# Performance work log

Hardware: AMD Instinct MI355X
Metric: run time of the kernel (lower is better)

Reference implementation:

```python
import jax, jax.numpy as jnp
import numpy as np

V, E, S_MAX, H, L = 32000, 1024, 2048, 16, 6
D = E // H  # head_dim = 64
EPS = 1e-5


def _ln(x, g, b):
    mu = jnp.mean(x, axis=-1, keepdims=True)
    var = jnp.mean(jnp.square(x - mu), axis=-1, keepdims=True)
    return (x - mu) * jax.lax.rsqrt(var + EPS) * g + b


def setup_inputs() -> dict:
    key = jax.random.key(0)
    ks = iter(jax.random.split(key, 32))
    std = 0.02
    B, S = 1, 2048
    inp = {
        "tokens": jax.random.randint(next(ks), (B, S), 0, V, dtype=jnp.int32),
        "W_emb": jax.random.normal(next(ks), (V, E), jnp.float32) * std,  # tied with fc_out
        "W_pos": jax.random.normal(next(ks), (S_MAX, E), jnp.float32) * std,
        # per-layer stacked params [L, ...]
        "Wq": jax.random.normal(next(ks), (L, E, E), jnp.float32) * std,
        "Wk": jax.random.normal(next(ks), (L, E, E), jnp.float32) * std,
        "Wv": jax.random.normal(next(ks), (L, E, E), jnp.float32) * std,
        "Wo": jax.random.normal(next(ks), (L, E, E), jnp.float32) * std,
        "bo": jnp.zeros((L, E), jnp.float32),
        "ln1_g": jnp.ones((L, E), jnp.float32),
        "ln1_b": jnp.zeros((L, E), jnp.float32),
        "ln2_g": jnp.ones((L, E), jnp.float32),
        "ln2_b": jnp.zeros((L, E), jnp.float32),
        "W1": jax.random.normal(next(ks), (L, 4 * E, E), jnp.float32) * std,
        "b1": jnp.zeros((L, 4 * E), jnp.float32),
        "W2": jax.random.normal(next(ks), (L, E, 4 * E), jnp.float32) * std,
        "b2": jnp.zeros((L, E), jnp.float32),
        "lnf_g": jnp.ones((E,), jnp.float32),
        "lnf_b": jnp.zeros((E,), jnp.float32),
    }
    return inp


def _gpt_forward(tokens, W_emb, W_pos, Wq, Wk, Wv, Wo, bo, ln1_g, ln1_b,
                 ln2_g, ln2_b, W1, b1, W2, b2, lnf_g, lnf_b):
    B, S = tokens.shape
    x = W_emb[tokens] + W_pos[:S][None, :, :]  # [B,S,E]
    causal = jnp.tril(jnp.ones((S, S), bool))  # [S,S]
    scale = 1.0 / np.sqrt(D)

    def block(x, p):
        wq, wk, wv, wo, bo_, g1, b1n, g2, b2n, w1, bf1, w2, bf2 = p
        h = _ln(x, g1, b1n)
        # torch Linear: y = x @ W.T ; split heads -> [B,H,S,D]
        def heads(w):
            return (h @ w.T).reshape(B, S, H, D).transpose(0, 2, 1, 3)
        q, k, v = heads(wq), heads(wk), heads(wv)
        scores = jnp.einsum('bhqd,bhkd->bhqk', q, k) * scale
        scores = jnp.where(causal[None, None], scores, -jnp.inf)
        attn = jax.nn.softmax(scores, axis=-1)
        o = jnp.einsum('bhqk,bhkd->bhqd', attn, v)
        o = o.transpose(0, 2, 1, 3).reshape(B, S, E)
        x = x + o @ wo.T + bo_
        h2 = _ln(x, g2, b2n)
        ff = jax.nn.gelu(h2 @ w1.T + bf1, approximate=False) @ w2.T + bf2
        return x + ff, None

    params = (Wq, Wk, Wv, Wo, bo, ln1_g, ln1_b, ln2_g, ln2_b, W1, b1, W2, b2)
    x, _ = jax.lax.scan(block, x, params)
    x = _ln(x, lnf_g, lnf_b)
    return x @ W_emb.T  # tied output projection [B,S,V]


def reference(tokens, W_emb, W_pos, Wq, Wk, Wv, Wo, bo, ln1_g, ln1_b,
              ln2_g, ln2_b, W1, b1, W2, b2, lnf_g, lnf_b):
    return _gpt_forward(tokens, W_emb, W_pos, Wq, Wk, Wv, Wo, bo, ln1_g,
                        ln1_b, ln2_g, ln2_b, W1, b1, W2, b2, lnf_g, lnf_b)
```

## Files before the change

### kernel.cpp

```cpp
#include <hip/hip_runtime.h>
#include <math.h>

#define S_LEN 2048
#define EMB 1024
#define NHEAD 16
#define HDIM 64
#define NLAYER 6
#define VOCAB 32000
#define FFDIM 4096

using f32x4 = __attribute__((ext_vector_type(4))) float;
using bf16x8 = __attribute__((ext_vector_type(8))) __bf16;
typedef unsigned short us;

static __device__ __forceinline__ unsigned short f2bf(float f) {
  union { float f; unsigned int u; } v; v.f = f;
  unsigned int r = v.u + 0x7FFFu + ((v.u >> 16) & 1u);
  return (unsigned short)(r >> 16);
}

#define GLOAD_LDS16(g, l)                                                      \
  __builtin_amdgcn_global_load_lds(                                            \
      (const __attribute__((address_space(1))) void*)(g),                      \
      (__attribute__((address_space(3))) void*)(l), 16, 0, 0)

__global__ __launch_bounds__(256) void cvt_bf16_kernel(
    const float* __restrict__ in, us* __restrict__ out, long n) {
  long i = ((long)blockIdx.x * 256 + threadIdx.x) * 8;
  if (i >= n) return;
  const float4* p = (const float4*)(in + i);
  float4 a = p[0], b = p[1];
  uint4 o;
  o.x = (unsigned)f2bf(a.x) | ((unsigned)f2bf(a.y) << 16);
  o.y = (unsigned)f2bf(a.z) | ((unsigned)f2bf(a.w) << 16);
  o.z = (unsigned)f2bf(b.x) | ((unsigned)f2bf(b.y) << 16);
  o.w = (unsigned)f2bf(b.z) | ((unsigned)f2bf(b.w) << 16);
  *(uint4*)(out + i) = o;
}

__global__ __launch_bounds__(256) void embed_kernel(
    const int* __restrict__ tok, const float* __restrict__ Wemb,
    const float* __restrict__ Wpos, float* __restrict__ x) {
  int s = blockIdx.x, t = threadIdx.x;
  int tk = tok[s];
  const float4* we = (const float4*)(Wemb + (size_t)tk * EMB);
  const float4* wp = (const float4*)(Wpos + (size_t)s * EMB);
  float4 a = we[t], b = wp[t];
  float4 o; o.x = a.x + b.x; o.y = a.y + b.y; o.z = a.z + b.z; o.w = a.w + b.w;
  ((float4*)(x + (size_t)s * EMB))[t] = o;
}

__global__ __launch_bounds__(256) void ln_kernel(
    const float* __restrict__ x, const float* __restrict__ g,
    const float* __restrict__ b, us* __restrict__ out) {
  int row = blockIdx.x, t = threadIdx.x, lane = t & 63, wave = t >> 6;
  float4 v = ((const float4*)(x + (size_t)row * EMB))[t];
  float s = v.x + v.y + v.z + v.w;
  float q = v.x * v.x + v.y * v.y + v.z * v.z + v.w * v.w;
  #pragma unroll
  for (int d = 1; d < 64; d <<= 1) { s += __shfl_xor(s, d); q += __shfl_xor(q, d); }
  __shared__ float rs[4], rq[4];
  if (lane == 0) { rs[wave] = s; rq[wave] = q; }
  __syncthreads();
  s = rs[0] + rs[1] + rs[2] + rs[3];
  q = rq[0] + rq[1] + rq[2] + rq[3];
  float mean = s * (1.0f / EMB);
  float var = q * (1.0f / EMB) - mean * mean;
  float rstd = rsqrtf(var + 1e-5f);
  float4 gg = ((const float4*)g)[t], bb = ((const float4*)b)[t];
  ushort4 o;
  o.x = f2bf((v.x - mean) * rstd * gg.x + bb.x);
  o.y = f2bf((v.y - mean) * rstd * gg.y + bb.y);
  o.z = f2bf((v.z - mean) * rstd * gg.z + bb.z);
  o.w = f2bf((v.w - mean) * rstd * gg.w + bb.w);
  ((ushort4*)(out + (size_t)row * EMB))[t] = o;
}

template <int SK>
__global__ __launch_bounds__(256) void reduce_ln_kernel(
    float* __restrict__ x, const float* __restrict__ p,
    const float* __restrict__ bias, const float* __restrict__ g,
    const float* __restrict__ b, us* __restrict__ out) {
  int row = blockIdx.x, t = threadIdx.x, lane = t & 63, wave = t >> 6;
  const size_t plane = (size_t)S_LEN * EMB;
  float4 v = ((const float4*)(x + (size_t)row * EMB))[t];
  float4 bb4 = ((const float4*)bias)[t];
  v.x += bb4.x; v.y += bb4.y; v.z += bb4.z; v.w += bb4.w;
  #pragma unroll
  for (int z = 0; z < SK; ++z) {
    float4 q4 = ((const float4*)(p + z * plane + (size_t)row * EMB))[t];
    v.x += q4.x; v.y += q4.y; v.z += q4.z; v.w += q4.w;
  }
  ((float4*)(x + (size_t)row * EMB))[t] = v;
  float s = v.x + v.y + v.z + v.w;
  float q = v.x * v.x + v.y * v.y + v.z * v.z + v.w * v.w;
  #pragma unroll
  for (int d = 1; d < 64; d <<= 1) { s += __shfl_xor(s, d); q += __shfl_xor(q, d); }
  __shared__ float rs[4], rq[4];
  if (lane == 0) { rs[wave] = s; rq[wave] = q; }
  __syncthreads();
  s = rs[0] + rs[1] + rs[2] + rs[3];
  q = rq[0] + rq[1] + rq[2] + rq[3];
  float mean = s * (1.0f / EMB);
  float var = q * (1.0f / EMB) - mean * mean;
  float rstd = rsqrtf(var + 1e-5f);
  float4 gg = ((const float4*)g)[t], lb = ((const float4*)b)[t];
  ushort4 o;
  o.x = f2bf((v.x - mean) * rstd * gg.x + lb.x);
  o.y = f2bf((v.y - mean) * rstd * gg.y + lb.y);
  o.z = f2bf((v.z - mean) * rstd * gg.z + lb.z);
  o.w = f2bf((v.w - mean) * rstd * gg.w + lb.w);
  ((ushort4*)(out + (size_t)row * EMB))[t] = o;
}

#define STAGE_R(MATP, BROW, LDSB, TT)                                          \
  {                                                                            \
    const int kk0 = (TT) << 5;                                                 \
    _Pragma("unroll")                                                          \
    for (int i_ = 0; i_ < 2; ++i_) {                                           \
      const int ci = t + i_ * 256;                                             \
      const int rr = ci >> 2, cc = ci & 3;                                     \
      const int src = (cc ^ ((rr >> 1) & 3)) * 8;                              \
      GLOAD_LDS16(MATP + (size_t)((BROW) + rr) * K + kk0 + src,                \
                  &LDSB[0] + (wave * 64 + i_ * 256) * 8);                      \
    }                                                                          \
  }

template <int HAS_BIAS, int DO_GELU, int OUT_BF16>
__global__ __launch_bounds__(256) void gemm_r128(
    const us* __restrict__ A, const us* __restrict__ B0,
    const us* __restrict__ B1, const us* __restrict__ B2,
    const float* __restrict__ bias,
    void* C0, void* C1, void* C2, int M, int N, int K) {
  const us* B = blockIdx.z == 0 ? B0 : (blockIdx.z == 1 ? B1 : B2);
  void* C = blockIdx.z == 0 ? C0 : (blockIdx.z == 1 ? C1 : C2);
  const int nwg = gridDim.x * gridDim.y;
  int lin = blockIdx.y * gridDim.x + blockIdx.x;
  {
    const int qx = nwg >> 3, r = nwg & 7;
    const int xcd = lin & 7, idx = lin >> 3;
    lin = (xcd < r ? xcd * (qx + 1) : r * (qx + 1) + (xcd - r) * qx) + idx;
  }
  const int m0 = (lin % gridDim.x) * 128, n0 = (lin / gridDim.x) * 128;
  const int t = threadIdx.x, lane = t & 63, wave = t >> 6;
  const int lq = lane & 15, hi = lane >> 4;
  const int wm = (wave >> 1) * 64, wn = (wave & 1) * 64;
  __shared__ __align__(16) us As[3][128 * 32];
  __shared__ __align__(16) us Bs[3][128 * 32];
  f32x4 acc[4][4] = {};
  const int nt = K >> 5;

  STAGE_R(A, m0, As[0], 0); STAGE_R(B, n0, Bs[0], 0);
  STAGE_R(A, m0, As[1], 1); STAGE_R(B, n0, Bs[1], 1);
  STAGE_R(A, m0, As[2], 2); STAGE_R(B, n0, Bs[2], 2);
  asm volatile("s_waitcnt vmcnt(8)" ::: "memory");
  __builtin_amdgcn_s_barrier();
  __builtin_amdgcn_sched_barrier(0);

  int bb = 0;
  for (int tt = 0; tt < nt; ++tt) {
    const int sb = (bb + 2 >= 3) ? bb - 1 : bb + 2;
    const us* Ab = &As[bb][0];
    const us* Bb = &Bs[bb][0];
    bf16x8 a[4], b[4];
    #pragma unroll
    for (int f = 0; f < 4; ++f) {
      const int row = wm + f * 16 + lq;
      a[f] = *(const bf16x8*)(Ab + row * 32 + ((hi ^ ((row >> 1) & 3)) * 8));
    }
    #pragma unroll
    for (int f = 0; f < 4; ++f) {
      const int row = wn + f * 16 + lq;
      b[f] = *(const bf16x8*)(Bb + row * 32 + ((hi ^ ((row >> 1) & 3)) * 8));
    }
    if (tt + 2 < nt) {
      STAGE_R(A, m0, As[sb], tt + 2);
      STAGE_R(B, n0, Bs[sb], tt + 2);
    }
    __builtin_amdgcn_s_setprio(1);
    #pragma unroll
    for (int i = 0; i < 4; ++i)
      #pragma unroll
      for (int j = 0; j < 4; ++j)
        acc[i][j] = __builtin_amdgcn_mfma_f32_16x16x32_bf16(a[i], b[j], acc[i][j], 0, 0, 0);
    __builtin_amdgcn_s_setprio(0);
    if (tt + 2 < nt) {
      asm volatile("s_waitcnt vmcnt(4)" ::: "memory");
    } else {
      asm volatile("s_waitcnt vmcnt(0)" ::: "memory");
    }
    __builtin_amdgcn_s_barrier();
    __builtin_amdgcn_sched_barrier(0);
    bb = (bb + 1 == 3) ? 0 : bb + 1;
  }
  const int r0 = hi * 4;
  #pragma unroll
  for (int i = 0; i < 4; ++i) {
    #pragma unroll
    for (int j = 0; j < 4; ++j) {
      const int col = n0 + wn + j * 16 + lq;
      float bv = HAS_BIAS ? bias[col] : 0.0f;
      #pragma unroll
      for (int r = 0; r < 4; ++r) {
        const int row = m0 + wm + i * 16 + r0 + r;
        float val = acc[i][j][r] + bv;
        if (DO_GELU) val = val * 0.5f * (1.0f + erff(val * 0.70710678118f));
        if (OUT_BF16) ((us*)C)[(size_t)row * N + col] = f2bf(val);
        else          ((float*)C)[(size_t)row * N + col] = val;
      }
    }
  }
}

__global__ __launch_bounds__(256) void gemm_rsk(
    const us* __restrict__ A, const us* __restrict__ B,
    float* __restrict__ C, int M, int N, int K, int kSlice) {
  const int z = blockIdx.z;
  const int nwg = gridDim.x * gridDim.y;
  int lin = blockIdx.y * gridDim.x + blockIdx.x;
  {
    const int qx = nwg >> 3, r = nwg & 7;
    const int xcd = lin & 7, idx = lin >> 3;
    lin = (xcd < r ? xcd * (qx + 1) : r * (qx + 1) + (xcd - r) * qx) + idx;
  }
  const int m0 = (lin % gridDim.x) * 128, n0 = (lin / gridDim.x) * 128;
  const int t = threadIdx.x, lane = t & 63, wave = t >> 6;
  const int lq = lane & 15, hi = lane >> 4;
  const int wm = (wave >> 1) * 64, wn = (wave & 1) * 64;
  __shared__ __align__(16) us As[3][128 * 32];
  __shared__ __align__(16) us Bs[3][128 * 32];
  f32x4 acc[4][4] = {};
  const int nt = kSlice >> 5;
  const int tb = z * (kSlice >> 5);

  STAGE_R(A, m0, As[0], tb + 0); STAGE_R(B, n0, Bs[0], tb + 0);
  STAGE_R(A, m0, As[1], tb + 1); STAGE_R(B, n0, Bs[1], tb + 1);
  STAGE_R(A, m0, As[2], tb + 2); STAGE_R(B, n0, Bs[2], tb + 2);
  asm volatile("s_waitcnt vmcnt(8)" ::: "memory");
  __builtin_amdgcn_s_barrier();
  __builtin_amdgcn_sched_barrier(0);

  int bb = 0;
  for (int tt = 0; tt < nt; ++tt) {
    const int sb = (bb + 2 >= 3) ? bb - 1 : bb + 2;
    const us* Ab = &As[bb][0];
    const us* Bb = &Bs[bb][0];
    bf16x8 a[4], b[4];
    #pragma unroll
    for (int f = 0; f < 4; ++f) {
      const int row = wm + f * 16 + lq;
      a[f] = *(const bf16x8*)(Ab + row * 32 + ((hi ^ ((row >> 1) & 3)) * 8));
    }
    #pragma unroll
    for (int f = 0; f < 4; ++f) {
      const int row = wn + f * 16 + lq;
      b[f] = *(const bf16x8*)(Bb + row * 32 + ((hi ^ ((row >> 1) & 3)) * 8));
    }
    if (tt + 2 < nt) {
      STAGE_R(A, m0, As[sb], tb + tt + 2);
      STAGE_R(B, n0, Bs[sb], tb + tt + 2);
    }
    __builtin_amdgcn_s_setprio(1);
    #pragma unroll
    for (int i = 0; i < 4; ++i)
      #pragma unroll
      for (int j = 0; j < 4; ++j)
        acc[i][j] = __builtin_amdgcn_mfma_f32_16x16x32_bf16(a[i], b[j], acc[i][j], 0, 0, 0);
    __builtin_amdgcn_s_setprio(0);
    if (tt + 2 < nt) {
      asm volatile("s_waitcnt vmcnt(4)" ::: "memory");
    } else {
      asm volatile("s_waitcnt vmcnt(0)" ::: "memory");
    }
    __builtin_amdgcn_s_barrier();
    __builtin_amdgcn_sched_barrier(0);
    bb = (bb + 1 == 3) ? 0 : bb + 1;
  }
  float* Cz = C + (size_t)z * M * N;
  #pragma unroll
  for (int i = 0; i < 4; ++i)
    #pragma unroll
    for (int j = 0; j < 4; ++j) {
      const int col = n0 + wn + j * 16 + lq;
      #pragma unroll
      for (int r = 0; r < 4; ++r)
        Cz[(size_t)(m0 + wm + i * 16 + hi * 4 + r) * N + col] = acc[i][j][r];
    }
}

__global__ __launch_bounds__(512, 1) void gemm_v8p(
    const us* __restrict__ A, const us* __restrict__ B,
    float* __restrict__ C, int M, int N, int K) {
  const int nwg = gridDim.x * gridDim.y;
  int lin = blockIdx.y * gridDim.x + blockIdx.x;
  {
    const int qx = nwg >> 3, r = nwg & 7;
    const int xcd = lin & 7, idx = lin >> 3;
    lin = (xcd < r ? xcd * (qx + 1) : r * (qx + 1) + (xcd - r) * qx) + idx;
  }
  const int m0 = (lin % gridDim.x) * 256, n0 = (lin / gridDim.x) * 256;
  const int t = threadIdx.x, lane = t & 63, wave = t >> 6;
  const int lq = lane & 15, hi = lane >> 4;
  const int rbase = (wave >> 2) * 128, cbase = (wave & 3) * 64;
  __shared__ __align__(16) us As[3][256 * 32];
  __shared__ __align__(16) us Bs[3][256 * 32];
  f32x4 acc[8][4] = {};
  const int nt = K >> 5;

#define STAGE_T(MAT, LDSB, TT)                                                 \
  {                                                                            \
    const int kk0 = (TT) << 5;                                                 \
    _Pragma("unroll")                                                          \
    for (int i_ = 0; i_ < 2; ++i_) {                                           \
      const int ci = t + i_ * 512;                                             \
      const int rr = ci >> 2, cc = ci & 3;                                     \
      const int src = (cc ^ ((rr >> 1) & 3)) * 8;                              \
      GLOAD_LDS16(MAT + (size_t)(((MAT == A) ? m0 : n0) + rr) * K + kk0 + src, \
                  &LDSB[0] + (wave * 64 + i_ * 512) * 8);                      \
    }                                                                          \
  }

  STAGE_T(A, As[0], 0); STAGE_T(B, Bs[0], 0);
  STAGE_T(A, As[1], 1); STAGE_T(B, Bs[1], 1);
  STAGE_T(A, As[2], 2); STAGE_T(B, Bs[2], 2);
  asm volatile("s_waitcnt vmcnt(8)" ::: "memory");
  __builtin_amdgcn_s_barrier();
  __builtin_amdgcn_sched_barrier(0);

  int bb = 0;
  for (int tt = 0; tt < nt; ++tt) {
    const int sb = (bb + 2 >= 3) ? bb - 1 : bb + 2;
    const us* Ab = &As[bb][0];
    const us* Bb = &Bs[bb][0];
    bf16x8 a0[4], a1[4], b0[4];
    #pragma unroll
    for (int f = 0; f < 4; ++f) {
      const int row = rbase + f * 16 + lq;
      a0[f] = *(const bf16x8*)(Ab + row * 32 + ((hi ^ ((row >> 1) & 3)) * 8));
    }
    #pragma unroll
    for (int f = 0; f < 4; ++f) {
      const int row = rbase + 64 + f * 16 + lq;
      a1[f] = *(const bf16x8*)(Ab + row * 32 + ((hi ^ ((row >> 1) & 3)) * 8));
    }
    #pragma unroll
    for (int f = 0; f < 4; ++f) {
      const int row = cbase + f * 16 + lq;
      b0[f] = *(const bf16x8*)(Bb + row * 32 + ((hi ^ ((row >> 1) & 3)) * 8));
    }
    if (tt + 2 < nt) {
      STAGE_T(A, As[sb], tt + 2);
      STAGE_T(B, Bs[sb], tt + 2);
    }
    __builtin_amdgcn_s_setprio(1);
    #pragma unroll
    for (int i = 0; i < 4; ++i)
      #pragma unroll
      for (int j = 0; j < 4; ++j)
        acc[i][j] = __builtin_amdgcn_mfma_f32_16x16x32_bf16(a0[i], b0[j], acc[i][j], 0, 0, 0);
    #pragma unroll
    for (int i = 0; i < 4; ++i)
      #pragma unroll
      for (int j = 0; j < 4; ++j)
        acc[4 + i][j] = __builtin_amdgcn_mfma_f32_16x16x32_bf16(a1[i], b0[j], acc[4 + i][j], 0, 0, 0);
    __builtin_amdgcn_s_setprio(0);
    if (tt + 2 < nt) {
      asm volatile("s_waitcnt vmcnt(4)" ::: "memory");
    } else {
      asm volatile("s_waitcnt vmcnt(0)" ::: "memory");
    }
    __builtin_amdgcn_s_barrier();
    __builtin_amdgcn_sched_barrier(0);
    bb = (bb + 1 == 3) ? 0 : bb + 1;
  }
#undef STAGE_T
  #pragma unroll
  for (int i = 0; i < 8; ++i)
    #pragma unroll
    for (int j = 0; j < 4; ++j) {
      const int col = n0 + cbase + j * 16 + lq;
      #pragma unroll
      for (int r = 0; r < 4; ++r)
        C[(size_t)(m0 + rbase + i * 16 + hi * 4 + r) * N + col] = acc[i][j][r];
    }
}

__global__ __launch_bounds__(256) void attn_kernel(
    const us* __restrict__ qb, const us* __restrict__ kb,
    const us* __restrict__ vb, us* __restrict__ ob) {
  const int qt = gridDim.x - 1 - blockIdx.x;
  const int head = blockIdx.y;
  const int t = threadIdx.x, lane = t & 63, wave = t >> 6;
  const int hi = lane >> 4, lq = lane & 15;
  const int hd = head * HDIM;
  const int q0w = qt * 64 + wave * 16;
  __shared__ __align__(16) us Kl[2][64 * 64];
  __shared__ __align__(16) us Vl[2][64 * 72];
  __shared__ __align__(16) us Pl[4][16][72];
  bf16x8 qf[2];
  {
    const us* qp = qb + (size_t)(q0w + lq) * EMB + hd + hi * 8;
    qf[0] = *(const bf16x8*)qp;
    qf[1] = *(const bf16x8*)(qp + 32);
    #pragma unroll
    for (int e = 0; e < 8; ++e) {
      qf[0][e] = (__bf16)((float)qf[0][e] * 0.125f);
      qf[1][e] = (__bf16)((float)qf[1][e] * 0.125f);
    }
  }
  f32x4 accO[4] = {};
  float m_run = -1e30f, l_run = 0.f;
  const int vr2 = (t >> 3) * 2, d8 = (t & 7) * 8;
  const int q_g = q0w + lq;

  {
    #pragma unroll
    for (int i = 0; i < 2; ++i) {
      const int c = wave * 64 + lane + i * 256;
      const int row = c >> 3, j = c & 7;
      const int colE = (j * 8) ^ ((row & 7) << 3);
      GLOAD_LDS16(kb + (size_t)(row) * EMB + hd + colE,
                  &Kl[0][0] + (wave * 64 + i * 256) * 8);
    }
    const us* vp = vb + (size_t)vr2 * EMB + hd + d8;
    uint4 vA = *(const uint4*)vp;
    uint4 vB = *(const uint4*)(vp + EMB);
    const unsigned* wa = (const unsigned*)&vA;
    const unsigned* wb = (const unsigned*)&vB;
    #pragma unroll
    for (int i = 0; i < 8; ++i) {
      unsigned lo = (i & 1) ? (wa[i >> 1] >> 16) : (wa[i >> 1] & 0xffffu);
      unsigned hw = (i & 1) ? (wb[i >> 1] >> 16) : (wb[i >> 1] & 0xffffu);
      *(unsigned*)(&Vl[0][0] + (d8 + i) * 72 + vr2) = lo | (hw << 16);
    }
  }
  __syncthreads();
  int cur = 0;
  for (int kt = 0; kt <= qt; ++kt) {
    uint4 vA, vB;
    if (kt < qt) {
      #pragma unroll
      for (int i = 0; i < 2; ++i) {
        const int c = wave * 64 + lane + i * 256;
        const int row = c >> 3, j = c & 7;
        const int colE = (j * 8) ^ ((row & 7) << 3);
        GLOAD_LDS16(kb + (size_t)((kt + 1) * 64 + row) * EMB + hd + colE,
                    &Kl[cur ^ 1][0] + (wave * 64 + i * 256) * 8);
      }
      const us* vp = vb + (size_t)((kt + 1) * 64 + vr2) * EMB + hd + d8;
      vA = *(const uint4*)vp;
      vB = *(const uint4*)(vp + EMB);
    }
    f32x4 sc[4] = {};
    #pragma unroll
    for (int ks = 0; ks < 2; ++ks) {
      #pragma unroll
      for (int fn = 0; fn < 4; ++fn) {
        const int rowk = fn * 16 + lq;
        const us* kp = &Kl[cur][0] + rowk * 64 + ((ks * 32 + hi * 8) ^ ((rowk & 7) << 3));
        sc[fn] = __builtin_amdgcn_mfma_f32_16x16x32_bf16(
            *(const bf16x8*)kp, qf[ks], sc[fn], 0, 0, 0);
      }
    }
    float pv[16];
    float pmax = -1e30f;
    if (kt == qt) {
      #pragma unroll
      for (int fn = 0; fn < 4; ++fn)
        #pragma unroll
        for (int r = 0; r < 4; ++r) {
          const int k_g = kt * 64 + fn * 16 + hi * 4 + r;
          float sv = sc[fn][r];
          if (k_g > q_g) sv = -1e30f;
          pv[fn * 4 + r] = sv;
          pmax = fmaxf(pmax, sv);
        }
    } else {
      #pragma unroll
      for (int fn = 0; fn < 4; ++fn)
        #pragma unroll
        for (int r = 0; r < 4; ++r) {
          float sv = sc[fn][r];
          pv[fn * 4 + r] = sv;
          pmax = fmaxf(pmax, sv);
        }
    }
    pmax = fmaxf(pmax, __shfl_xor(pmax, 16));
    pmax = fmaxf(pmax, __shfl_xor(pmax, 32));
    if (!__all(pmax <= m_run + 8.0f)) {
      const float mn = fmaxf(m_run, pmax);
      const float alpha = __expf(m_run - mn);
      m_run = mn;
      l_run *= alpha;
      float ar[4];
      #pragma unroll
      for (int r = 0; r < 4; ++r) ar[r] = __shfl(alpha, hi * 4 + r);
      #pragma unroll
      for (int df = 0; df < 4; ++df)
        #pragma unroll
        for (int r = 0; r < 4; ++r) accO[df][r] *= ar[r];
    }
    float rsum = 0.f;
    #pragma unroll
    for (int i = 0; i < 16; ++i) {
      float e = __expf(pv[i] - m_run);
      pv[i] = e;
      rsum += e;
    }
    rsum += __shfl_xor(rsum, 16);
    rsum += __shfl_xor(rsum, 32);
    l_run += rsum;
    #pragma unroll
    for (int fn = 0; fn < 4; ++fn) {
      ushort4 pk;
      pk.x = f2bf(pv[fn * 4 + 0]);
      pk.y = f2bf(pv[fn * 4 + 1]);
      pk.z = f2bf(pv[fn * 4 + 2]);
      pk.w = f2bf(pv[fn * 4 + 3]);
      *(ushort4*)&Pl[wave][lq][fn * 16 + hi * 4] = pk;
    }
    #pragma unroll
    for (int ks = 0; ks < 2; ++ks) {
      bf16x8 pf = *(const bf16x8*)&Pl[wave][lq][ks * 32 + hi * 8];
      #pragma unroll
      for (int df = 0; df < 4; ++df) {
        bf16x8 vf = *(const bf16x8*)(&Vl[cur][0] + (df * 16 + lq) * 72 + ks * 32 + hi * 8);
        accO[df] = __builtin_amdgcn_mfma_f32_16x16x32_bf16(pf, vf, accO[df], 0, 0, 0);
      }
    }
    if (kt < qt) {
      const unsigned* wa = (const unsigned*)&vA;
      const unsigned* wb = (const unsigned*)&vB;
      #pragma unroll
      for (int i = 0; i < 8; ++i) {
        unsigned lo = (i & 1) ? (wa[i >> 1] >> 16) : (wa[i >> 1] & 0xffffu);
        unsigned hw = (i & 1) ? (wb[i >> 1] >> 16) : (wb[i >> 1] & 0xffffu);
        *(unsigned*)(&Vl[cur ^ 1][0] + (d8 + i) * 72 + vr2) = lo | (hw << 16);
      }
    }
    __syncthreads();
    cur ^= 1;
  }
  float linv[4];
  #pragma unroll
  for (int r = 0; r < 4; ++r) linv[r] = 1.0f / __shfl(l_run, hi * 4 + r);
  #pragma unroll
  for (int r = 0; r < 4; ++r) {
    const int row = q0w + hi * 4 + r;
    #pragma unroll
    for (int df = 0; df < 4; ++df)
      ob[(size_t)row * EMB + hd + df * 16 + lq] = f2bf(accO[df][r] * linv[r]);
  }
}

extern "C" void kernel_launch(void* const* d_in, const int* in_sizes, int n_in,
                              void* d_out, int out_size, void* d_ws, size_t ws_size,
                              hipStream_t stream) {
  const int* tok = (const int*)d_in[0];
  const float* Wemb = (const float*)d_in[1];
  const float* Wpos = (const float*)d_in[2];
  const float* Wq = (const float*)d_in[3];
  const float* Wk = (const float*)d_in[4];
  const float* Wv = (const float*)d_in[5];
  const float* Wo = (const float*)d_in[6];
  const float* bo = (const float*)d_in[7];
  const float* ln1g = (const float*)d_in[8];
  const float* ln1b = (const float*)d_in[9];
  const float* ln2g = (const float*)d_in[10];
  const float* ln2b = (const float*)d_in[11];
  const float* W1 = (const float*)d_in[12];
  const float* b1 = (const float*)d_in[13];
  const float* W2 = (const float*)d_in[14];
  const float* b2 = (const float*)d_in[15];
  const float* lnfg = (const float*)d_in[16];
  const float* lnfb = (const float*)d_in[17];
  (void)in_sizes; (void)n_in; (void)out_size;

  const size_t MB = 1u << 20;
  char* ws = (char*)d_ws;
  float* x = (float*)ws;
  us* h  = (us*)(ws + 8 * MB);
  us* qb = (us*)(ws + 12 * MB);
  us* kb = (us*)(ws + 16 * MB);
  us* vb = (us*)(ws + 20 * MB);
  us* ob = (us*)(ws + 24 * MB);
  us* fb = (us*)(ws + 12 * MB);
  us* cWq = (us*)(ws + 28 * MB);
  us* cWk = (us*)(ws + 40 * MB);
  us* cWv = (us*)(ws + 52 * MB);
  us* cWo = (us*)(ws + 64 * MB);
  us* cW1 = (us*)(ws + 76 * MB);
  us* cW2 = (us*)(ws + 124 * MB);
  us* cWemb = (us*)(ws + 172 * MB);
  float* pbuf = (float*)(ws + 236 * MB);
  const size_t need = 236 * MB + 32 * MB;
  if (ws_size < need) {
    embed_kernel<<<dim3(S_LEN), 256, 0, stream>>>(tok, Wemb, Wpos, x);
    return;
  }

  embed_kernel<<<dim3(S_LEN), 256, 0, stream>>>(tok, Wemb, Wpos, x);

  const long nE2 = (long)NLAYER * EMB * EMB;
  const long nF  = (long)NLAYER * FFDIM * EMB;
  const long nV  = (long)VOCAB * EMB;
  cvt_bf16_kernel<<<(int)(nE2 / 2048), 256, 0, stream>>>(Wq, cWq, nE2);
  cvt_bf16_kernel<<<(int)(nE2 / 2048), 256, 0, stream>>>(Wk, cWk, nE2);
  cvt_bf16_kernel<<<(int)(nE2 / 2048), 256, 0, stream>>>(Wv, cWv, nE2);
  cvt_bf16_kernel<<<(int)(nE2 / 2048), 256, 0, stream>>>(Wo, cWo, nE2);
  cvt_bf16_kernel<<<(int)(nF / 2048), 256, 0, stream>>>(W1, cW1, nF);
  cvt_bf16_kernel<<<(int)(nF / 2048), 256, 0, stream>>>(W2, cW2, nF);
  cvt_bf16_kernel<<<(int)(nV / 2048), 256, 0, stream>>>(Wemb, cWemb, nV);

  ln_kernel<<<S_LEN, 256, 0, stream>>>(x, ln1g, ln1b, h);
  for (int l = 0; l < NLAYER; ++l) {
    const size_t wofs = (size_t)l * EMB * EMB;
    const size_t fofs = (size_t)l * FFDIM * EMB;
    gemm_r128<0, 0, 1><<<dim3(16, 8, 3), 256, 0, stream>>>(
        h, cWq + wofs, cWk + wofs, cWv + wofs, nullptr,
        qb, kb, vb, S_LEN, EMB, EMB);
    attn_kernel<<<dim3(32, NHEAD), 256, 0, stream>>>(qb, kb, vb, ob);
    gemm_rsk<<<dim3(16, 8, 2), 256, 0, stream>>>(
        ob, cWo + wofs, pbuf, S_LEN, EMB, EMB, EMB / 2);
    reduce_ln_kernel<2><<<S_LEN, 256, 0, stream>>>(
        x, pbuf, bo + l * EMB, ln2g + l * EMB, ln2b + l * EMB, h);
    gemm_r128<1, 1, 1><<<dim3(16, 32, 1), 256, 0, stream>>>(
        h, cW1 + fofs, nullptr, nullptr, b1 + l * FFDIM,
        fb, nullptr, nullptr, S_LEN, FFDIM, EMB);
    gemm_rsk<<<dim3(16, 8, 4), 256, 0, stream>>>(
        fb, cW2 + fofs, pbuf, S_LEN, EMB, FFDIM, FFDIM / 4);
    if (l < NLAYER - 1)
      reduce_ln_kernel<4><<<S_LEN, 256, 0, stream>>>(
          x, pbuf, b2 + l * EMB, ln1g + (l + 1) * EMB, ln1b + (l + 1) * EMB, h);
    else
      reduce_ln_kernel<4><<<S_LEN, 256, 0, stream>>>(
          x, pbuf, b2 + l * EMB, lnfg, lnfb, h);
  }
  gemm_v8p<<<dim3(8, 125), 512, 0, stream>>>(
      h, cWemb, (float*)d_out, S_LEN, VOCAB, EMB);
}
```

Before: 1.382 ms.

## Add 64-row QKV GEMM, use exp2 softmax, split Wo GEMM four ways

Adds a new gemm_r64 kernel with 64x128 tiles for the QKV projection, doubling the grid from 384 to 768 workgroups to fill the CUs better. In attention, the log2(e) factor is folded into the Q prescale so softmax can use exp2f instead of __expf. The Wo projection's split-K goes from 2 to 4 slices, with the matching reduce_ln variant. These aim to raise occupancy and parallelism, at the cost of more partial-sum traffic and less reuse per tile.

```diff
diff --git a/kernel.cpp b/kernel.cpp
--- a/kernel.cpp
+++ b/kernel.cpp
@@ -210,6 +210,107 @@
       }
     }
   }
+}
+
+__global__ __launch_bounds__(256) void gemm_r64(
+    const us* __restrict__ A, const us* __restrict__ B0,
+    const us* __restrict__ B1, const us* __restrict__ B2,
+    void* C0, void* C1, void* C2, int M, int N, int K) {
+  const us* B = blockIdx.z == 0 ? B0 : (blockIdx.z == 1 ? B1 : B2);
+  void* C = blockIdx.z == 0 ? C0 : (blockIdx.z == 1 ? C1 : C2);
+  const int nwg = gridDim.x * gridDim.y;
+  int lin = blockIdx.y * gridDim.x + blockIdx.x;
+  {
+    const int qx = nwg >> 3, r = nwg & 7;
+    const int xcd = lin & 7, idx = lin >> 3;
+    lin = (xcd < r ? xcd * (qx + 1) : r * (qx + 1) + (xcd - r) * qx) + idx;
+  }
+  const int m0 = (lin % gridDim.x) * 64, n0 = (lin / gridDim.x) * 128;
+  const int t = threadIdx.x, lane = t & 63, wave = t >> 6;
+  const int lq = lane & 15, hi = lane >> 4;
+  const int wm = (wave >> 1) * 32, wn = (wave & 1) * 64;
+  __shared__ __align__(16) us As[3][64 * 32];
+  __shared__ __align__(16) us Bs[3][128 * 32];
+  f32x4 acc[2][4] = {};
+  const int nt = K >> 5;
+
+#define STAGE_A64(LDSB, TT)                                                    \
+  {                                                                            \
+    const int kk0 = (TT) << 5;                                                 \
+    const int rr = t >> 2, cc = t & 3;                                         \
+    const int src = (cc ^ ((rr >> 1) & 3)) * 8;                                \
+    GLOAD_LDS16(A + (size_t)(m0 + rr) * K + kk0 + src,                         \
+                &LDSB[0] + (wave * 64) * 8);                                   \
+  }
+#define STAGE_B64(LDSB, TT)                                                    \
+  {                                                                            \
+    const int kk0 = (TT) << 5;                                                 \
+    _Pragma("unroll")                                                          \
+    for (int i_ = 0; i_ < 2; ++i_) {                                           \
+      const int ci = t + i_ * 256;                                             \
+      const int rr = ci >> 2, cc = ci & 3;                                     \
+      const int src = (cc ^ ((rr >> 1) & 3)) * 8;                              \
+      GLOAD_LDS16(B + (size_t)(n0 + rr) * K + kk0 + src,                       \
+                  &LDSB[0] + (wave * 64 + i_ * 256) * 8);                      \
+    }                                                                          \
+  }
+
+  STAGE_A64(As[0], 0); STAGE_B64(Bs[0], 0);
+  STAGE_A64(As[1], 1); STAGE_B64(Bs[1], 1);
+  STAGE_A64(As[2], 2); STAGE_B64(Bs[2], 2);
+  asm volatile("s_waitcnt vmcnt(6)" ::: "memory");
+  __builtin_amdgcn_s_barrier();
+  __builtin_amdgcn_sched_barrier(0);
+
+  int bb = 0;
+  for (int tt = 0; tt < nt; ++tt) {
+    const int sb = (bb + 2 >= 3) ? bb - 1 : bb + 2;
+    const us* Ab = &As[bb][0];
+    const us* Bb = &Bs[bb][0];
+    bf16x8 a[2], b[4];
+    #pragma unroll
+    for (int f = 0; f < 2; ++f) {
+      const int row = wm + f * 16 + lq;
+      a[f] = *(const bf16x8*)(Ab + row * 32 + ((hi ^ ((row >> 1) & 3)) * 8));
+    }
+    #pragma unroll
+    for (int f = 0; f < 4; ++f) {
+      const int row = wn + f * 16 + lq;
+      b[f] = *(const bf16x8*)(Bb + row * 32 + ((hi ^ ((row >> 1) & 3)) * 8));
+    }
+    if (tt + 2 < nt) {
+      STAGE_A64(As[sb], tt + 2);
+      STAGE_B64(Bs[sb], tt + 2);
+    }
+    __builtin_amdgcn_s_setprio(1);
+    #pragma unroll
+    for (int i = 0; i < 2; ++i)
+      #pragma unroll
+      for (int j = 0; j < 4; ++j)
+        acc[i][j] = __builtin_amdgcn_mfma_f32_16x16x32_bf16(a[i], b[j], acc[i][j], 0, 0, 0);
+    __builtin_amdgcn_s_setprio(0);
+    if (tt + 2 < nt) {
+      asm volatile("s_waitcnt vmcnt(3)" ::: "memory");
+    } else {
+      asm volatile("s_waitcnt vmcnt(0)" ::: "memory");
+    }
+    __builtin_amdgcn_s_barrier();
+    __builtin_amdgcn_sched_barrier(0);
+    bb = (bb + 1 == 3) ? 0 : bb + 1;
+  }
+#undef STAGE_A64
+#undef STAGE_B64
+  #pragma unroll
+  for (int i = 0; i < 2; ++i)
+    #pragma unroll
+    for (int j = 0; j < 4; ++j) {
+      const int col = n0 + wn + j * 16 + lq;
+      #pragma unroll
+      for (int r = 0; r < 4; ++r) {
+        const int row = m0 + wm + i * 16 + hi * 4 + r;
+        ((us*)C)[(size_t)row * N + col] = f2bf(acc[i][j][r]);
+      }
+    }
 }
 
 __global__ __launch_bounds__(256) void gemm_rsk(
@@ -404,8 +505,8 @@
     qf[1] = *(const bf16x8*)(qp + 32);
     #pragma unroll
     for (int e = 0; e < 8; ++e) {
-      qf[0][e] = (__bf16)((float)qf[0][e] * 0.125f);
-      qf[1][e] = (__bf16)((float)qf[1][e] * 0.125f);
+      qf[0][e] = (__bf16)((float)qf[0][e] * 0.18033688f);
+      qf[1][e] = (__bf16)((float)qf[1][e] * 0.18033688f);
     }
   }
   f32x4 accO[4] = {};
@@ -489,7 +590,7 @@
     pmax = fmaxf(pmax, __shfl_xor(pmax, 32));
     if (!__all(pmax <= m_run + 8.0f)) {
       const float mn = fmaxf(m_run, pmax);
-      const float alpha = __expf(m_run - mn);
+      const float alpha = exp2f(m_run - mn);
       m_run = mn;
       l_run *= alpha;
       float ar[4];
@@ -503,7 +604,7 @@
     float rsum = 0.f;
     #pragma unroll
     for (int i = 0; i < 16; ++i) {
-      float e = __expf(pv[i] - m_run);
+      float e = exp2f(pv[i] - m_run);
       pv[i] = e;
       rsum += e;
     }
@@ -616,13 +717,13 @@
   for (int l = 0; l < NLAYER; ++l) {
     const size_t wofs = (size_t)l * EMB * EMB;
     const size_t fofs = (size_t)l * FFDIM * EMB;
-    gemm_r128<0, 0, 1><<<dim3(16, 8, 3), 256, 0, stream>>>(
-        h, cWq + wofs, cWk + wofs, cWv + wofs, nullptr,
+    gemm_r64<<<dim3(32, 8, 3), 256, 0, stream>>>(
+        h, cWq + wofs, cWk + wofs, cWv + wofs,
         qb, kb, vb, S_LEN, EMB, EMB);
     attn_kernel<<<dim3(32, NHEAD), 256, 0, stream>>>(qb, kb, vb, ob);
-    gemm_rsk<<<dim3(16, 8, 2), 256, 0, stream>>>(
-        ob, cWo + wofs, pbuf, S_LEN, EMB, EMB, EMB / 2);
-    reduce_ln_kernel<2><<<S_LEN, 256, 0, stream>>>(
+    gemm_rsk<<<dim3(16, 8, 4), 256, 0, stream>>>(
+        ob, cWo + wofs, pbuf, S_LEN, EMB, EMB, EMB / 4);
+    reduce_ln_kernel<4><<<S_LEN, 256, 0, stream>>>(
         x, pbuf, bo + l * EMB, ln2g + l * EMB, ln2b + l * EMB, h);
     gemm_r128<1, 1, 1><<<dim3(16, 32, 1), 256, 0, stream>>>(
         h, cW1 + fofs, nullptr, nullptr, b1 + l * FFDIM,
```

Measured after the change: 1.418 ms. 2.6% more time.
